# Kernel tuning notes

Hardware: AMD Instinct MI355X
Metric: run time of the kernel (lower is better)

The kernel has to match this reference:

```python
import jax, jax.numpy as jnp
import numpy as np

EMB = 128
N_RBF = 16
N_EDGES = 1_000_000
N_ATOMS = 50_000


def setup_inputs() -> dict:
    key = jax.random.key(0)
    ks = jax.random.split(key, 16)
    inp = {
        "x": jax.random.normal(ks[0], (N_EDGES, EMB), dtype=jnp.float32),
        "rbf": jax.random.normal(ks[1], (N_EDGES, N_RBF), dtype=jnp.float32),
        "idnb_i": jax.random.randint(ks[2], (N_EDGES,), 0, N_ATOMS, dtype=jnp.int32),
        "n_atoms": N_ATOMS,
        # learned params
        "W_x": jax.random.normal(ks[3], (EMB, EMB), dtype=jnp.float32) * 0.05,
        "b_x": jnp.zeros((EMB,), dtype=jnp.float32),
        "W_rbf": jax.random.normal(ks[4], (N_RBF, EMB), dtype=jnp.float32) * 0.2,
        "b_rbf": jnp.zeros((EMB,), dtype=jnp.float32),
        "W1": jax.random.normal(ks[5], (EMB, EMB), dtype=jnp.float32) * 0.05,
        "b1": jnp.zeros((EMB,), dtype=jnp.float32),
        "W2": jax.random.normal(ks[6], (EMB, EMB), dtype=jnp.float32) * 0.05,
        "b2": jnp.zeros((EMB,), dtype=jnp.float32),
        "W3": jax.random.normal(ks[7], (EMB, EMB), dtype=jnp.float32) * 0.05,
        "b3": jnp.zeros((EMB,), dtype=jnp.float32),
        "W_final": jax.random.normal(ks[8], (EMB, 1), dtype=jnp.float32) * 0.05,
        # scale coefficients (shape [1] as in the keras layer)
        "coef_rbf_a": jnp.exp(jax.random.normal(ks[9], (1,)) * 0.01),
        "coef_rbf_b": jnp.exp(jax.random.normal(ks[10], (1,)) * 0.01),
        "coef_x": jnp.exp(jax.random.normal(ks[11], (1,)) * 0.01),
        "coef_final": jnp.exp(jax.random.normal(ks[12], (1,)) * 0.01),
    }
    return inp


def reference(x, rbf, idnb_i, n_atoms, W_x, b_x, W_rbf, b_rbf, W1, b1, W2, b2,
              W3, b3, W_final, coef_rbf_a, coef_rbf_b, coef_x, coef_final):
    act = jax.nn.silu  # keras 'swish'
    rbf = coef_rbf_a * rbf
    h = act(x @ W_x + b_x)                      # [E, emb]
    g = act(rbf @ W_rbf + b_rbf)                # [E, emb]
    conv_x = (coef_rbf_b * g) * (coef_x * h)    # fused elementwise gate
    a = jax.ops.segment_sum(conv_x, idnb_i, num_segments=n_atoms)  # [n_atoms, emb]
    a = act(a @ W1 + b1)
    a = act(a @ W2 + b2)
    a = act(a @ W3 + b3)
    out = (a @ W_final) * coef_final            # [n_atoms, 1]
    return out
```

## Files before the change

kernel.cpp:

```cpp
#include <hip/hip_runtime.h>

#define E_TOTAL 1000000
#define EMB     128
#define NRBF    16
#define NATOMS  50000
#define APB     40
#define NBLK    ((NATOMS + 255) / 256)

typedef _Float16 f16x8 __attribute__((ext_vector_type(8)));
typedef _Float16 f16x4 __attribute__((ext_vector_type(4)));
typedef float    f32x4 __attribute__((ext_vector_type(4)));

__device__ __forceinline__ float silu_f(float v) {
    return v * (1.0f / (1.0f + __expf(-v)));
}

__device__ __forceinline__ int sigma64(int e) {
    return (((e & 15) >> 2) << 4) + ((e >> 4) << 2) + (e & 3);
}

__global__ __launch_bounds__(256)
void hist_kernel(const int* __restrict__ idnb, int* __restrict__ counts) {
    const int e = blockIdx.x * 256 + threadIdx.x;
    if (e < E_TOTAL) atomicAdd(&counts[idnb[e]], 1);
}

__global__ __launch_bounds__(256)
void scan1_kernel(const int* __restrict__ counts, int* __restrict__ row_ptr,
                  int* __restrict__ bsums) {
    __shared__ int sd[256];
    const int tid = threadIdx.x;
    const int idx = blockIdx.x * 256 + tid;
    const int v = (idx < NATOMS) ? counts[idx] : 0;
    sd[tid] = v;
    __syncthreads();
#pragma unroll
    for (int off = 1; off < 256; off <<= 1) {
        const int t = (tid >= off) ? sd[tid - off] : 0;
        __syncthreads();
        sd[tid] += t;
        __syncthreads();
    }
    if (idx < NATOMS) row_ptr[idx] = sd[tid] - v;
    if (tid == 255) bsums[blockIdx.x] = sd[255];
}

__global__ __launch_bounds__(256)
void scan2_kernel(int* __restrict__ bsums) {
    __shared__ int sd[256];
    const int tid = threadIdx.x;
    const int v = (tid < NBLK) ? bsums[tid] : 0;
    sd[tid] = v;
    __syncthreads();
#pragma unroll
    for (int off = 1; off < 256; off <<= 1) {
        const int t = (tid >= off) ? sd[tid - off] : 0;
        __syncthreads();
        sd[tid] += t;
        __syncthreads();
    }
    if (tid < NBLK) bsums[tid] = sd[tid] - v;
}

__global__ __launch_bounds__(256)
void scan3_kernel(const int* __restrict__ bsums, int* __restrict__ row_ptr,
                  int* __restrict__ cursor) {
    const int idx = blockIdx.x * 256 + threadIdx.x;
    if (idx < NATOMS) {
        const int r = row_ptr[idx] + bsums[blockIdx.x];
        row_ptr[idx] = r;
        cursor[idx]  = r;
    }
    if (idx == 0) row_ptr[NATOMS] = E_TOTAL;
}

__global__ __launch_bounds__(256)
void scatter_kernel(const int* __restrict__ idnb, int* __restrict__ cursor,
                    int* __restrict__ eidx) {
    const int e = blockIdx.x * 256 + threadIdx.x;
    if (e < E_TOTAL) {
        const int a = idnb[e];
        const int p = atomicAdd(&cursor[a], 1);
        eidx[p] = e;
    }
}

__global__ __launch_bounds__(256, 2)
void edge_kernel(const float* __restrict__ x,
                 const float* __restrict__ rbf,
                 const int*   __restrict__ eidx,
                 const int*   __restrict__ row_ptr,
                 const float* __restrict__ Wx,
                 const float* __restrict__ bx,
                 const float* __restrict__ Wr,
                 const float* __restrict__ br,
                 const float* __restrict__ c_a,
                 const float* __restrict__ c_b,
                 const float* __restrict__ c_x,
                 float* __restrict__ acc)
{
    __shared__ _Float16 sX[64 * 128];
    __shared__ _Float16 sR[64 * 40];
    __shared__ float    sAcc[APB][132];
    __shared__ int      sAid[64];

    const int tid  = threadIdx.x;
    const int w    = tid >> 6;
    const int lane = tid & 63;
    const int lq   = lane >> 4;
    const int lm   = lane & 15;

    const int aBase = blockIdx.x * APB;

    int rp[APB];
#pragma unroll
    for (int a = 0; a < APB; ++a) rp[a] = row_ptr[aBase + a];
    const int eBeg = rp[0];
    const int eEnd = row_ptr[aBase + APB];
    const int nEdge = eEnd - eBeg;
    const int ntile = (nEdge + 63) >> 6;

    const float ca = c_a[0];
    const float sc = c_b[0] * c_x[0];
    const int col0 = w * 32 + lm;
    const int col1 = col0 + 16;
    const float bx0 = bx[col0], bx1 = bx[col1];
    const float br0 = br[col0], br1 = br[col1];

    f16x8 wxh[4][2], wxl[4][2], wrh[2], wrl[2];
#pragma unroll
    for (int ks = 0; ks < 4; ++ks)
#pragma unroll
        for (int nt = 0; nt < 2; ++nt) {
            const int n = w * 32 + nt * 16 + lm;
            f16x8 h8, l8;
#pragma unroll
            for (int j = 0; j < 8; ++j) {
                const int k = ks * 32 + lq * 8 + j;
                const float v = Wx[k * EMB + n];
                const _Float16 hv = (_Float16)v;
                h8[j] = hv;
                l8[j] = (_Float16)(v - (float)hv);
            }
            wxh[ks][nt] = h8;
            wxl[ks][nt] = l8;
        }
#pragma unroll
    for (int nt = 0; nt < 2; ++nt) {
        const int n = w * 32 + nt * 16 + lm;
        f16x8 h8, l8;
#pragma unroll
        for (int j = 0; j < 8; ++j) {
            const int k = lq * 8 + j;
            const float v = (k < NRBF) ? Wr[k * EMB + n] : 0.f;
            const _Float16 hv = (_Float16)v;
            h8[j] = hv;
            l8[j] = (_Float16)(v - (float)hv);
        }
        wrh[nt] = h8;
        wrl[nt] = l8;
    }

    for (int f = tid; f < APB * 132; f += 256) ((float*)sAcc)[f] = 0.f;
    for (int f = tid; f < 64 * 24; f += 256)
        sR[(f / 24) * 40 + 16 + (f % 24)] = (_Float16)0.f;

    float4 px[8];
    float4 pr;
    int    prel = -1;

    auto prefetch = [&](int t) {
        const int nb = eBeg + t * 64;
#pragma unroll
        for (int i = 0; i < 8; ++i) {
            const int e = (tid >> 5) + i * 8;
            const int eid = eidx[min(nb + sigma64(e), eEnd - 1)];
            px[i] = *(const float4*)(x + (size_t)eid * EMB + (tid & 31) * 4);
        }
        {
            const int er = tid >> 2;
            const int eid = eidx[min(nb + sigma64(er), eEnd - 1)];
            pr = *(const float4*)(rbf + (size_t)eid * NRBF + (tid & 3) * 4);
        }
        if (tid < 64) {
            const int pos = nb + tid;
            if (pos >= eEnd) {
                prel = -1;
            } else {
                int rel = 0;
#pragma unroll
                for (int a = 1; a < APB; ++a) rel += (pos >= rp[a]) ? 1 : 0;
                prel = rel;
            }
        }
    };

    auto write_lds = [&]() {
#pragma unroll
        for (int i = 0; i < 8; ++i) {
            const int e = (tid >> 5) + i * 8;
            const int kb = (tid & 31) * 4;
            const int idx = (e * 128 + kb) ^ ((e & 7) << 3);
            f16x4 h4 = {(_Float16)px[i].x, (_Float16)px[i].y,
                        (_Float16)px[i].z, (_Float16)px[i].w};
            *(f16x4*)&sX[idx] = h4;
        }
        {
            const int er = tid >> 2;
            const int kb = (tid & 3) * 4;
            f16x4 r4 = {(_Float16)(pr.x * ca), (_Float16)(pr.y * ca),
                        (_Float16)(pr.z * ca), (_Float16)(pr.w * ca)};
            *(f16x4*)&sR[er * 40 + kb] = r4;
        }
        if (tid < 64) sAid[tid] = prel;
    };

    if (ntile > 0) prefetch(0);

    for (int t = 0; t < ntile; ++t) {
        __syncthreads();
        write_lds();
        __syncthreads();
        if (t + 1 < ntile) prefetch(t + 1);

        int   curA = -2;
        float a0v = 0.f, a1v = 0.f;

        auto epi = [&](const f32x4 hac[2], const f32x4 gac[2], int mt) {
            const int pbase = lq * 16 + mt * 4;
            float v0[4], v1[4];
#pragma unroll
            for (int r = 0; r < 4; ++r) {
                const float g0 = gac[0][r] + br0, h0 = hac[0][r] + bx0;
                const float g1 = gac[1][r] + br1, h1 = hac[1][r] + bx1;
                const float d0 = (1.f + __expf(-g0)) * (1.f + __expf(-h0));
                const float d1 = (1.f + __expf(-g1)) * (1.f + __expf(-h1));
                v0[r] = sc * g0 * h0 * __builtin_amdgcn_rcpf(d0);
                v1[r] = sc * g1 * h1 * __builtin_amdgcn_rcpf(d1);
            }
#pragma unroll
            for (int r = 0; r < 4; ++r) {
                const int rel = sAid[pbase + r];
                if (rel != curA) {
                    if (curA >= 0) {
                        atomicAdd(&sAcc[curA][col0], a0v);
                        atomicAdd(&sAcc[curA][col1], a1v);
                    }
                    curA = rel; a0v = 0.f; a1v = 0.f;
                }
                a0v += v0[r];
                a1v += v1[r];
            }
        };

        auto mfma_mt = [&](f32x4 hac[2], f32x4 gac[2], int mt) {
#pragma unroll
            for (int nt = 0; nt < 2; ++nt) { hac[nt] = 0.f; gac[nt] = 0.f; }
            const int m = mt * 16 + lm;
            const f16x8 rh = *(const f16x8*)&sR[m * 40 + lq * 8];
#pragma unroll
            for (int nt = 0; nt < 2; ++nt) {
                gac[nt] = __builtin_amdgcn_mfma_f32_16x16x32_f16(rh, wrh[nt], gac[nt], 0, 0, 0);
                gac[nt] = __builtin_amdgcn_mfma_f32_16x16x32_f16(rh, wrl[nt], gac[nt], 0, 0, 0);
            }
#pragma unroll
            for (int ks = 0; ks < 4; ++ks) {
                const int xi = (m * 128 + ks * 32 + lq * 8) ^ ((m & 7) << 3);
                const f16x8 xh = *(const f16x8*)&sX[xi];
#pragma unroll
                for (int nt = 0; nt < 2; ++nt) {
                    hac[nt] = __builtin_amdgcn_mfma_f32_16x16x32_f16(xh, wxh[ks][nt], hac[nt], 0, 0, 0);
                    hac[nt] = __builtin_amdgcn_mfma_f32_16x16x32_f16(xh, wxl[ks][nt], hac[nt], 0, 0, 0);
                }
            }
        };

#pragma unroll
        for (int g = 0; g < 2; ++g) {
            f32x4 hacA[2], gacA[2], hacB[2], gacB[2];
            mfma_mt(hacA, gacA, g * 2);
            mfma_mt(hacB, gacB, g * 2 + 1);
            epi(hacA, gacA, g * 2);
            epi(hacB, gacB, g * 2 + 1);
        }

        if (curA >= 0) {
            atomicAdd(&sAcc[curA][col0], a0v);
            atomicAdd(&sAcc[curA][col1], a1v);
        }
    }

    __syncthreads();
#pragma unroll
    for (int it = 0; it < 3; ++it) {
        const int r = (tid >> 4) + it * 16;
        if (r < APB) {
            const int c = (tid & 15) * 8;
            float* dst = acc + (size_t)(aBase + r) * EMB + c;
            *(float4*)(dst)     = *(const float4*)&sAcc[r][c];
            *(float4*)(dst + 4) = *(const float4*)&sAcc[r][c + 4];
        }
    }
}

__global__ __launch_bounds__(256, 2)
void mlp_fused_kernel(const float* __restrict__ X,
                      const float* __restrict__ W1, const float* __restrict__ b1,
                      const float* __restrict__ W2, const float* __restrict__ b2,
                      const float* __restrict__ W3, const float* __restrict__ b3,
                      const float* __restrict__ Wf, const float* __restrict__ cf,
                      float* __restrict__ out, int M)
{
    __shared__ _Float16 sA[128 * 128];
    __shared__ _Float16 sB[128 * 128];
    __shared__ float    sOut[128];

    const int tid  = threadIdx.x;
    const int w    = tid >> 6;
    const int lane = tid & 63;
    const int lq   = lane >> 4;
    const int lm   = lane & 15;

    const int base = blockIdx.x * 128;
    const int col0 = w * 32 + lm;
    const int col1 = col0 + 16;
    const float wf0 = Wf[col0], wf1 = Wf[col1];
    const float cfv = cf[0];

    if (tid < 128) sOut[tid] = 0.f;

#pragma unroll
    for (int i = 0; i < 16; ++i) {
        const int e = (tid >> 5) + i * 8;
        const int row = min(base + e, M - 1);
        const float4 v = *(const float4*)(X + (size_t)row * EMB + (tid & 31) * 4);
        const int kb = (tid & 31) * 4;
        const int idx = (e * 128 + kb) ^ ((e & 7) << 3);
        f16x4 h4 = {(_Float16)v.x, (_Float16)v.y, (_Float16)v.z, (_Float16)v.w};
        *(f16x4*)&sA[idx] = h4;
    }
    __syncthreads();

    const float* Ws[3] = {W1, W2, W3};
    const float* bs[3] = {b1, b2, b3};

#pragma unroll 1
    for (int L = 0; L < 3; ++L) {
        const _Float16* sIn   = (L & 1) ? sB : sA;
        _Float16*       sDst  = (L & 1) ? sA : sB;
        const float*    W     = Ws[L];
        const float     bb0   = bs[L][col0];
        const float     bb1   = bs[L][col1];

        f16x8 wh[4][2], wl[4][2];
#pragma unroll
        for (int ks = 0; ks < 4; ++ks)
#pragma unroll
            for (int nt = 0; nt < 2; ++nt) {
                const int n = w * 32 + nt * 16 + lm;
                f16x8 h8, l8;
#pragma unroll
                for (int j = 0; j < 8; ++j) {
                    const int k = ks * 32 + lq * 8 + j;
                    const float v = W[k * EMB + n];
                    const _Float16 hv = (_Float16)v;
                    h8[j] = hv;
                    l8[j] = (_Float16)(v - (float)hv);
                }
                wh[ks][nt] = h8;
                wl[ks][nt] = l8;
            }

#pragma unroll
        for (int sub = 0; sub < 2; ++sub) {
#pragma unroll
            for (int mth = 0; mth < 2; ++mth) {
                f32x4 hac[2][2];
#pragma unroll
                for (int mi = 0; mi < 2; ++mi)
#pragma unroll
                    for (int nt = 0; nt < 2; ++nt) hac[mi][nt] = 0.f;

#pragma unroll
                for (int mi = 0; mi < 2; ++mi) {
                    const int m = sub * 64 + (mth * 2 + mi) * 16 + lm;
#pragma unroll
                    for (int ks = 0; ks < 4; ++ks) {
                        const int xi = (m * 128 + ks * 32 + lq * 8) ^ ((m & 7) << 3);
                        const f16x8 xh = *(const f16x8*)&sIn[xi];
#pragma unroll
                        for (int nt = 0; nt < 2; ++nt) {
                            hac[mi][nt] = __builtin_amdgcn_mfma_f32_16x16x32_f16(xh, wh[ks][nt], hac[mi][nt], 0, 0, 0);
                            hac[mi][nt] = __builtin_amdgcn_mfma_f32_16x16x32_f16(xh, wl[ks][nt], hac[mi][nt], 0, 0, 0);
                        }
                    }
                }

#pragma unroll
                for (int mi = 0; mi < 2; ++mi) {
                    const int rowl = sub * 64 + (mth * 2 + mi) * 16 + lq * 4;
                    if (L < 2) {
#pragma unroll
                        for (int r = 0; r < 4; ++r) {
                            const float o0 = silu_f(hac[mi][0][r] + bb0);
                            const float o1 = silu_f(hac[mi][1][r] + bb1);
                            const int rw = rowl + r;
                            sDst[(rw * 128 + col0) ^ ((rw & 7) << 3)] = (_Float16)o0;
                            sDst[(rw * 128 + col1) ^ ((rw & 7) << 3)] = (_Float16)o1;
                        }
                    } else {
#pragma unroll
                        for (int r = 0; r < 4; ++r) {
                            const float o0 = silu_f(hac[mi][0][r] + bb0);
                            const float o1 = silu_f(hac[mi][1][r] + bb1);
                            float p = o0 * wf0 + o1 * wf1;
#pragma unroll
                            for (int off = 1; off < 16; off <<= 1)
                                p += __shfl_xor(p, off);
                            if (lm == 0 && base + rowl + r < M)
                                atomicAdd(&sOut[rowl + r], p);
                        }
                    }
                }
            }
        }
        __syncthreads();
    }

    if (tid < 128) {
        const int row = base + tid;
        if (row < M) out[row] = sOut[tid] * cfv;
    }
}

extern "C" void kernel_launch(void* const* d_in, const int* in_sizes, int n_in,
                              void* d_out, int out_size, void* d_ws, size_t ws_size,
                              hipStream_t stream) {
    const float* x    = (const float*)d_in[0];
    const float* rbf  = (const float*)d_in[1];
    const int*   idnb = (const int*)  d_in[2];
    const float* Wx   = (const float*)d_in[4];
    const float* bx   = (const float*)d_in[5];
    const float* Wr   = (const float*)d_in[6];
    const float* brf  = (const float*)d_in[7];
    const float* W1   = (const float*)d_in[8];
    const float* b1   = (const float*)d_in[9];
    const float* W2   = (const float*)d_in[10];
    const float* b2   = (const float*)d_in[11];
    const float* W3   = (const float*)d_in[12];
    const float* b3   = (const float*)d_in[13];
    const float* Wf   = (const float*)d_in[14];
    const float* c_a  = (const float*)d_in[15];
    const float* c_b  = (const float*)d_in[16];
    const float* c_x  = (const float*)d_in[17];
    const float* c_f  = (const float*)d_in[18];

    float* out = (float*)d_out;
    float* acc = (float*)d_ws;
    float* buf = acc + (size_t)NATOMS * EMB;
    int* eidx    = (int*)buf;
    int* counts  = eidx + E_TOTAL;
    int* row_ptr = counts + NATOMS;
    int* cursor  = row_ptr + NATOMS + 1;
    int* bsums   = cursor + NATOMS;

    hipMemsetAsync(counts, 0, NATOMS * sizeof(int), stream);

    hist_kernel<<<(E_TOTAL + 255) / 256, 256, 0, stream>>>(idnb, counts);
    scan1_kernel<<<NBLK, 256, 0, stream>>>(counts, row_ptr, bsums);
    scan2_kernel<<<1, 256, 0, stream>>>(bsums);
    scan3_kernel<<<NBLK, 256, 0, stream>>>(bsums, row_ptr, cursor);
    scatter_kernel<<<(E_TOTAL + 255) / 256, 256, 0, stream>>>(idnb, cursor, eidx);

    edge_kernel<<<NATOMS / APB, 256, 0, stream>>>(x, rbf, eidx, row_ptr,
                                                  Wx, bx, Wr, brf,
                                                  c_a, c_b, c_x, acc);

    mlp_fused_kernel<<<(NATOMS + 127) / 128, 256, 0, stream>>>(
        acc, W1, b1, W2, b2, W3, b3, Wf, c_f, out, NATOMS);
}
```

Baseline: 380.1 us.

## Load edge rows directly into MFMA registers and cache edge/atom indices in LDS

Removes the LDS staging of x and rbf tiles. Each wave now loads the x and rbf rows it needs for its MFMA A-operand straight from global memory, double-buffered across the four m-tiles. The scatter kernel also writes a sorted atom-index array, and the edge kernel caches up to 1536 edge and atom indices per block in LDS. This replaces the per-edge 40-way row_ptr comparison and the two block barriers per tile. In exchange every wave loads its own copy of the rows with less coalesced 32-byte accesses per lane, register pressure rises, and the scatter kernel does an extra 4 MB write.

```diff
diff --git a/kernel.cpp b/kernel.cpp
--- a/kernel.cpp
+++ b/kernel.cpp
@@ -6,6 +6,7 @@
 #define NATOMS  50000
 #define APB     40
 #define NBLK    ((NATOMS + 255) / 256)
+#define ECACHE  1536
 
 typedef _Float16 f16x8 __attribute__((ext_vector_type(8)));
 typedef _Float16 f16x4 __attribute__((ext_vector_type(4)));
@@ -13,10 +14,6 @@
 
 __device__ __forceinline__ float silu_f(float v) {
     return v * (1.0f / (1.0f + __expf(-v)));
-}
-
-__device__ __forceinline__ int sigma64(int e) {
-    return (((e & 15) >> 2) << 4) + ((e >> 4) << 2) + (e & 3);
 }
 
 __global__ __launch_bounds__(256)
@@ -76,12 +73,13 @@
 
 __global__ __launch_bounds__(256)
 void scatter_kernel(const int* __restrict__ idnb, int* __restrict__ cursor,
-                    int* __restrict__ eidx) {
+                    int* __restrict__ eidx, int* __restrict__ aidxs) {
     const int e = blockIdx.x * 256 + threadIdx.x;
     if (e < E_TOTAL) {
         const int a = idnb[e];
         const int p = atomicAdd(&cursor[a], 1);
-        eidx[p] = e;
+        eidx[p]  = e;
+        aidxs[p] = a;
     }
 }
 
@@ -89,6 +87,7 @@
 void edge_kernel(const float* __restrict__ x,
                  const float* __restrict__ rbf,
                  const int*   __restrict__ eidx,
+                 const int*   __restrict__ aidxs,
                  const int*   __restrict__ row_ptr,
                  const float* __restrict__ Wx,
                  const float* __restrict__ bx,
@@ -99,10 +98,9 @@
                  const float* __restrict__ c_x,
                  float* __restrict__ acc)
 {
-    __shared__ _Float16 sX[64 * 128];
-    __shared__ _Float16 sR[64 * 40];
-    __shared__ float    sAcc[APB][132];
-    __shared__ int      sAid[64];
+    __shared__ float sAcc[APB][132];
+    __shared__ int   sEid[ECACHE];
+    __shared__ int   sAid[ECACHE];
 
     const int tid  = threadIdx.x;
     const int w    = tid >> 6;
@@ -111,12 +109,8 @@
     const int lm   = lane & 15;
 
     const int aBase = blockIdx.x * APB;
-
-    int rp[APB];
-#pragma unroll
-    for (int a = 0; a < APB; ++a) rp[a] = row_ptr[aBase + a];
-    const int eBeg = rp[0];
-    const int eEnd = row_ptr[aBase + APB];
+    const int eBeg  = row_ptr[aBase];
+    const int eEnd  = row_ptr[aBase + APB];
     const int nEdge = eEnd - eBeg;
     const int ntile = (nEdge + 63) >> 6;
 
@@ -162,72 +156,90 @@
     }
 
     for (int f = tid; f < APB * 132; f += 256) ((float*)sAcc)[f] = 0.f;
-    for (int f = tid; f < 64 * 24; f += 256)
-        sR[(f / 24) * 40 + 16 + (f % 24)] = (_Float16)0.f;
-
-    float4 px[8];
-    float4 pr;
-    int    prel = -1;
-
-    auto prefetch = [&](int t) {
+    for (int f = tid; f < ECACHE; f += 256) {
+        const bool in = (f < nEdge);
+        sEid[f] = in ? eidx[eBeg + f]  : 0;
+        sAid[f] = in ? aidxs[eBeg + f] : -1;
+    }
+    __syncthreads();
+
+    auto lookup_eid = [&](int p) -> int {
+        const int off = p - eBeg;
+        return (off < ECACHE) ? sEid[off] : eidx[p];
+    };
+
+    auto issue_mt = [&](int nb, int mt, float4 (&px)[8], float4 (&pr)[2],
+                        int& relbase_eid) {
+        const int pA = min(nb + ((lm >> 2) << 4) + (mt << 2) + (lm & 3), eEnd - 1);
+        const int eid = lookup_eid(pA);
+        relbase_eid = eid;
+        const float* xr = x + (size_t)eid * EMB;
+#pragma unroll
+        for (int ks = 0; ks < 4; ++ks) {
+            px[2 * ks]     = *(const float4*)(xr + ks * 32 + lq * 8);
+            px[2 * ks + 1] = *(const float4*)(xr + ks * 32 + lq * 8 + 4);
+        }
+        if (lq < 2) {
+            const float* rr = rbf + (size_t)eid * NRBF + lq * 8;
+            pr[0] = *(const float4*)(rr);
+            pr[1] = *(const float4*)(rr + 4);
+        }
+    };
+
+    for (int t = 0; t < ntile; ++t) {
         const int nb = eBeg + t * 64;
-#pragma unroll
-        for (int i = 0; i < 8; ++i) {
-            const int e = (tid >> 5) + i * 8;
-            const int eid = eidx[min(nb + sigma64(e), eEnd - 1)];
-            px[i] = *(const float4*)(x + (size_t)eid * EMB + (tid & 31) * 4);
-        }
-        {
-            const int er = tid >> 2;
-            const int eid = eidx[min(nb + sigma64(er), eEnd - 1)];
-            pr = *(const float4*)(rbf + (size_t)eid * NRBF + (tid & 3) * 4);
-        }
-        if (tid < 64) {
-            const int pos = nb + tid;
-            if (pos >= eEnd) {
-                prel = -1;
-            } else {
-                int rel = 0;
-#pragma unroll
-                for (int a = 1; a < APB; ++a) rel += (pos >= rp[a]) ? 1 : 0;
-                prel = rel;
-            }
-        }
-    };
-
-    auto write_lds = [&]() {
-#pragma unroll
-        for (int i = 0; i < 8; ++i) {
-            const int e = (tid >> 5) + i * 8;
-            const int kb = (tid & 31) * 4;
-            const int idx = (e * 128 + kb) ^ ((e & 7) << 3);
-            f16x4 h4 = {(_Float16)px[i].x, (_Float16)px[i].y,
-                        (_Float16)px[i].z, (_Float16)px[i].w};
-            *(f16x4*)&sX[idx] = h4;
-        }
-        {
-            const int er = tid >> 2;
-            const int kb = (tid & 3) * 4;
-            f16x4 r4 = {(_Float16)(pr.x * ca), (_Float16)(pr.y * ca),
-                        (_Float16)(pr.z * ca), (_Float16)(pr.w * ca)};
-            *(f16x4*)&sR[er * 40 + kb] = r4;
-        }
-        if (tid < 64) sAid[tid] = prel;
-    };
-
-    if (ntile > 0) prefetch(0);
-
-    for (int t = 0; t < ntile; ++t) {
-        __syncthreads();
-        write_lds();
-        __syncthreads();
-        if (t + 1 < ntile) prefetch(t + 1);
+
+        float4 pxE[8], pxO[8];
+        float4 prE[2], prO[2];
+        int eidE, eidO;
+
+        issue_mt(nb, 0, pxE, prE, eidE);
 
         int   curA = -2;
         float a0v = 0.f, a1v = 0.f;
 
-        auto epi = [&](const f32x4 hac[2], const f32x4 gac[2], int mt) {
-            const int pbase = lq * 16 + mt * 4;
+#pragma unroll
+        for (int mt = 0; mt < 4; ++mt) {
+            if (mt == 0) issue_mt(nb, 1, pxO, prO, eidO);
+            else if (mt == 1) issue_mt(nb, 2, pxE, prE, eidE);
+            else if (mt == 2) issue_mt(nb, 3, pxO, prO, eidO);
+
+            const float4 (&px)[8] = (mt & 1) ? pxO : pxE;
+            const float4 (&pr)[2] = (mt & 1) ? prO : prE;
+
+            f32x4 hac[2], gac[2];
+#pragma unroll
+            for (int nt = 0; nt < 2; ++nt) { hac[nt] = 0.f; gac[nt] = 0.f; }
+
+            f16x8 rh;
+            if (lq < 2) {
+                rh = f16x8{(_Float16)(pr[0].x * ca), (_Float16)(pr[0].y * ca),
+                           (_Float16)(pr[0].z * ca), (_Float16)(pr[0].w * ca),
+                           (_Float16)(pr[1].x * ca), (_Float16)(pr[1].y * ca),
+                           (_Float16)(pr[1].z * ca), (_Float16)(pr[1].w * ca)};
+            } else {
+                rh = f16x8{(_Float16)0.f, (_Float16)0.f, (_Float16)0.f, (_Float16)0.f,
+                           (_Float16)0.f, (_Float16)0.f, (_Float16)0.f, (_Float16)0.f};
+            }
+#pragma unroll
+            for (int nt = 0; nt < 2; ++nt) {
+                gac[nt] = __builtin_amdgcn_mfma_f32_16x16x32_f16(rh, wrh[nt], gac[nt], 0, 0, 0);
+                gac[nt] = __builtin_amdgcn_mfma_f32_16x16x32_f16(rh, wrl[nt], gac[nt], 0, 0, 0);
+            }
+
+#pragma unroll
+            for (int ks = 0; ks < 4; ++ks) {
+                const float4 a = px[2 * ks];
+                const float4 b = px[2 * ks + 1];
+                const f16x8 xh = {(_Float16)a.x, (_Float16)a.y, (_Float16)a.z, (_Float16)a.w,
+                                  (_Float16)b.x, (_Float16)b.y, (_Float16)b.z, (_Float16)b.w};
+#pragma unroll
+                for (int nt = 0; nt < 2; ++nt) {
+                    hac[nt] = __builtin_amdgcn_mfma_f32_16x16x32_f16(xh, wxh[ks][nt], hac[nt], 0, 0, 0);
+                    hac[nt] = __builtin_amdgcn_mfma_f32_16x16x32_f16(xh, wxl[ks][nt], hac[nt], 0, 0, 0);
+                }
+            }
+
             float v0[4], v1[4];
 #pragma unroll
             for (int r = 0; r < 4; ++r) {
@@ -240,7 +252,15 @@
             }
 #pragma unroll
             for (int r = 0; r < 4; ++r) {
-                const int rel = sAid[pbase + r];
+                const int p = nb + (lq << 4) + (mt << 2) + r;
+                int rel;
+                if (p >= eEnd) {
+                    rel = -1;
+                } else {
+                    const int off = p - eBeg;
+                    const int a = (off < ECACHE) ? sAid[off] : aidxs[p];
+                    rel = a - aBase;
+                }
                 if (rel != curA) {
                     if (curA >= 0) {
                         atomicAdd(&sAcc[curA][col0], a0v);
@@ -251,39 +271,7 @@
                 a0v += v0[r];
                 a1v += v1[r];
             }
-        };
-
-        auto mfma_mt = [&](f32x4 hac[2], f32x4 gac[2], int mt) {
-#pragma unroll
-            for (int nt = 0; nt < 2; ++nt) { hac[nt] = 0.f; gac[nt] = 0.f; }
-            const int m = mt * 16 + lm;
-            const f16x8 rh = *(const f16x8*)&sR[m * 40 + lq * 8];
-#pragma unroll
-            for (int nt = 0; nt < 2; ++nt) {
-                gac[nt] = __builtin_amdgcn_mfma_f32_16x16x32_f16(rh, wrh[nt], gac[nt], 0, 0, 0);
-                gac[nt] = __builtin_amdgcn_mfma_f32_16x16x32_f16(rh, wrl[nt], gac[nt], 0, 0, 0);
-            }
-#pragma unroll
-            for (int ks = 0; ks < 4; ++ks) {
-                const int xi = (m * 128 + ks * 32 + lq * 8) ^ ((m & 7) << 3);
-                const f16x8 xh = *(const f16x8*)&sX[xi];
-#pragma unroll
-                for (int nt = 0; nt < 2; ++nt) {
-                    hac[nt] = __builtin_amdgcn_mfma_f32_16x16x32_f16(xh, wxh[ks][nt], hac[nt], 0, 0, 0);
-                    hac[nt] = __builtin_amdgcn_mfma_f32_16x16x32_f16(xh, wxl[ks][nt], hac[nt], 0, 0, 0);
-                }
-            }
-        };
-
-#pragma unroll
-        for (int g = 0; g < 2; ++g) {
-            f32x4 hacA[2], gacA[2], hacB[2], gacB[2];
-            mfma_mt(hacA, gacA, g * 2);
-            mfma_mt(hacB, gacB, g * 2 + 1);
-            epi(hacA, gacA, g * 2);
-            epi(hacB, gacB, g * 2 + 1);
-        }
-
+        }
         if (curA >= 0) {
             atomicAdd(&sAcc[curA][col0], a0v);
             atomicAdd(&sAcc[curA][col1], a1v);
@@ -459,7 +447,8 @@
     float* acc = (float*)d_ws;
     float* buf = acc + (size_t)NATOMS * EMB;
     int* eidx    = (int*)buf;
-    int* counts  = eidx + E_TOTAL;
+    int* aidxs   = eidx + E_TOTAL;
+    int* counts  = aidxs + E_TOTAL;
     int* row_ptr = counts + NATOMS;
     int* cursor  = row_ptr + NATOMS + 1;
     int* bsums   = cursor + NATOMS;
@@ -470,9 +459,9 @@
     scan1_kernel<<<NBLK, 256, 0, stream>>>(counts, row_ptr, bsums);
     scan2_kernel<<<1, 256, 0, stream>>>(bsums);
     scan3_kernel<<<NBLK, 256, 0, stream>>>(bsums, row_ptr, cursor);
-    scatter_kernel<<<(E_TOTAL + 255) / 256, 256, 0, stream>>>(idnb, cursor, eidx);
-
-    edge_kernel<<<NATOMS / APB, 256, 0, stream>>>(x, rbf, eidx, row_ptr,
+    scatter_kernel<<<(E_TOTAL + 255) / 256, 256, 0, stream>>>(idnb, cursor, eidx, aidxs);
+
+    edge_kernel<<<NATOMS / APB, 256, 0, stream>>>(x, rbf, eidx, aidxs, row_ptr,
                                                   Wx, bx, Wr, brf,
                                                   c_a, c_b, c_x, acc);
 
```

Measured after the change: 486.8 us. 28.1% more time.
